# Optimization experiments

Measured on AMD Instinct MI355X. Metric: run time of the kernel, lower is better.

## Reference

```python
import jax, jax.numpy as jnp
from jax import lax
import numpy as np

H_AA = 20          # raw Potts alphabet
H_PAD = 22         # after (0,2) pad on both residue axes
EMB = H_PAD * H_PAD  # 484, LightAttention channel dim == MLP width
KSZ = 9            # LightAttention conv kernel


def setup_inputs() -> dict:
    key = jax.random.key(0)
    ks = jax.random.split(key, 16)
    b, n, k = 8, 512, 30
    S_mut = 99
    sc = 0.02
    inp = {
        'batch_etab': jax.random.normal(ks[0], (b, n, k, H_AA * H_AA), dtype=jnp.float32),
        'E_idx': jax.random.randint(ks[1], (b, n, k), 0, n),
        'sortcery_seqs': jax.random.randint(ks[2], (b, S_mut, n), 0, H_AA),
        'seqs': jax.random.randint(ks[3], (b, n), 0, H_AA),
        'mut_pos': jax.random.randint(ks[4], (b,), 0, n),
        'nodes': jnp.zeros((1,), dtype=jnp.float32),
        # LightAttention params (Conv1d: [out_ch, in_ch, ksz])
        'W_f': jax.random.normal(ks[5], (EMB, EMB, KSZ), dtype=jnp.float32) * sc,
        'b_f': jnp.zeros((EMB,), dtype=jnp.float32),
        'W_a': jax.random.normal(ks[6], (EMB, EMB, KSZ), dtype=jnp.float32) * sc,
        'b_a': jnp.zeros((EMB,), dtype=jnp.float32),
        # both_out: ReLU -> Linear(EMB,EMB) -> ReLU -> Linear(EMB,484)
        'W1': jax.random.normal(ks[7], (EMB, EMB), dtype=jnp.float32) * sc,
        'b1': jnp.zeros((EMB,), dtype=jnp.float32),
        'W2': jax.random.normal(ks[8], (EMB, EMB), dtype=jnp.float32) * sc,
        'b2': jnp.zeros((EMB,), dtype=jnp.float32),
        # ddg_out: Linear(1,1) -> scalar affine
        'w_ddg': jax.random.normal(ks[9], (1, 1), dtype=jnp.float32),
        'b_ddg': jnp.zeros((1,), dtype=jnp.float32),
    }
    return inp


def _conv1d_same(x, W, b):
    # x: [B, C, L], W: [O, I, K] -> [B, O, L] (stride 1, SAME pad for K=9)
    p = KSZ // 2
    y = lax.conv_general_dilated(x, W, (1,), [(p, p)],
                                 dimension_numbers=('NCH', 'OIH', 'NCH'))
    return y + b[None, :, None]


def reference(batch_etab, E_idx, sortcery_seqs, seqs, mut_pos, nodes,
              W_f, b_f, W_a, b_a, W1, b1, W2, b2, w_ddg, b_ddg):
    b, n, k, hh = batch_etab.shape
    h = H_AA
    # view (b,n,k,h,h), pad last two dims (0,2) each, flatten -> (b,n,k,484)
    e = batch_etab.reshape(b, n, k, h, h)
    e = jnp.pad(e, ((0, 0), (0, 0), (0, 0), (0, 2), (0, 2)))
    e = e.reshape(b, n, k, EMB)

    bidx = jnp.arange(b)
    # expand_etab_4d followed by [mut_pos] row-select == scatter the mut_pos
    # neighbor slab into a dense [n, EMB] row (avoids the full [n,n,EMB] dense).
    rows = e[bidx, mut_pos]          # [b, k, EMB]
    nbrs = E_idx[bidx, mut_pos]      # [b, k]
    lin = jnp.zeros((b, n, EMB), dtype=batch_etab.dtype)
    lin = lin.at[bidx[:, None], nbrs].set(rows)   # [b, n, EMB]

    mask = lin[:, :, 0] != 0                       # [b, n]

    # LightAttention (eval mode: dropout = identity)
    x = lin.transpose(0, 2, 1)                     # [b, EMB, n]
    o = _conv1d_same(x, W_f, b_f)
    att = _conv1d_same(x, W_a, b_a)
    att = jnp.where(mask[:, None, :], att, -1e9)
    o1 = o * jax.nn.softmax(att, axis=-1)          # [b, EMB, n]
    la = o1.transpose(0, 2, 1)                     # [b, n, EMB]

    # both_out: ReLU -> Linear -> ReLU -> Linear
    y = jax.nn.relu(la) @ W1.T + b1
    y = jax.nn.relu(y) @ W2.T + b2                 # [b, n, 484]
    # ddg_out Linear(1,1) applied elementwise on trailing singleton
    ddg = y * w_ddg[0, 0] + b_ddg[0]               # [b, n, 484]

    etab2 = ddg.reshape(b, n, H_PAD, H_PAD)        # [b, n, 22, 22]

    sort_seqs = jnp.concatenate([sortcery_seqs, seqs[:, None, :]], axis=1)  # [b,S,n]
    S = sort_seqs.shape[1]
    # batch_score_seq_batch_pos: score[b,s] = sum_j etab2[b, j, seq[mut_pos], seq[j]]
    s_pos = jnp.take_along_axis(sort_seqs, mut_pos[:, None, None], axis=2)[..., 0]  # [b,S]
    scores = etab2[bidx[:, None, None], jnp.arange(n)[None, None, :],
                   s_pos[:, :, None], sort_seqs].sum(axis=-1)  # [b, S]

    # subtract WT (last) score, drop WT row
    all_scores = (scores - scores[:, -1:])[:, :-1]             # [b, S-1]
    return all_scores
```

## Files before the change

### kernel.cpp

```cpp
#include <hip/hip_runtime.h>
#include <math.h>

#define H_AA   20
#define H_PAD  22
#define EMB    484
#define KSZ    9
#define NB     8
#define NPOS   512
#define KNBR   30
#define SMUT   99
#define STOT   100
#define ROWS   (NB*KNBR)
#define MROWS  241
#define NTOT   968
#define KC     400

__global__ void setup_kernel(const int* __restrict__ E_idx,
                             const int* __restrict__ mut_pos,
                             const float* __restrict__ etab,
                             int* __restrict__ rowidx_g,
                             int* __restrict__ mcount,
                             int* __restrict__ pairtap,
                             int* __restrict__ cnttap) {
    int b  = blockIdx.x;
    int mp = mut_pos[b];
    __shared__ int jmap[NPOS];
    __shared__ int wcnt[8], wbase[8];
    int t = threadIdx.x;
    jmap[t] = -1;
    __syncthreads();
    if (t < KNBR) {
        int nb = E_idx[(b * NPOS + mp) * KNBR + t];
        bool winner = true;
        for (int j2 = t + 1; j2 < KNBR; ++j2)
            if (E_idx[(b * NPOS + mp) * KNBR + j2] == nb) { winner = false; break; }
        if (winner) jmap[nb] = t;
    }
    __syncthreads();
    int j = jmap[t];
    int f = 0;
    if (j >= 0) {
        float c0 = etab[(((size_t)(b * NPOS + mp)) * KNBR + j) * 400];
        f = (c0 != 0.0f) ? 1 : 0;
    }
    unsigned long long bal = __ballot(f);
    int lane = t & 63, w = t >> 6;
    if (lane == 0) wcnt[w] = __popcll(bal);
    __syncthreads();
    if (t == 0) {
        int s = 0;
        for (int ww = 0; ww < 8; ++ww) { wbase[ww] = s; s += wcnt[ww]; }
        mcount[b] = s;
    }
    __syncthreads();
    int ridx = -1;
    if (f) ridx = wbase[w] + __popcll(bal & ((1ull << lane) - 1ull));
    rowidx_g[b * NPOS + t] = ridx;
    if (f) {
        int row = b * KNBR + ridx;
        for (int d = -4; d <= 4; ++d) {
            int q = t + d;
            if (q < 0 || q >= NPOS) continue;
            int jq = jmap[q];
            if (jq < 0) continue;
            int tap = d + 4;
            int idx = atomicAdd(&cnttap[tap], 1);
            pairtap[tap * 256 + idx] = (row << 5) | jq;
        }
    }
}

__global__ void pack_conv_kernel(const float* __restrict__ Wf,
                                 const float* __restrict__ Wa,
                                 float* __restrict__ Wp) {
    int half = blockIdx.z;
    const float* src = half ? Wa : Wf;
    int cb = blockIdx.x * 32;
    int ob = blockIdx.y * 32;
    __shared__ float tile[32][33];
    for (int yy = threadIdx.y; yy < 32; yy += 8) {
        int out = ob + yy, c = cb + threadIdx.x;
        if (out < EMB && c < EMB * KSZ)
            tile[yy][threadIdx.x] = src[(size_t)out * (EMB * KSZ) + c];
    }
    __syncthreads();
    for (int yy = threadIdx.y; yy < 32; yy += 8) {
        int c = cb + yy, out = ob + threadIdx.x;
        if (c < EMB * KSZ && out < EMB) {
            int tap = c % 9, in_pad = c / 9;
            int rr = in_pad / H_PAD, cc = in_pad % H_PAD;
            if (rr < H_AA && cc < H_AA) {
                int k = tap * KC + rr * H_AA + cc;
                Wp[(size_t)k * NTOT + half * EMB + out] = tile[threadIdx.x][yy];
            }
        }
    }
}

__global__ void transpose_lin_kernel(const float* __restrict__ W1,
                                     const float* __restrict__ W2,
                                     float* __restrict__ W1t,
                                     float* __restrict__ W2t) {
    const float* src = blockIdx.z ? W2 : W1;
    float*       dst = blockIdx.z ? W2t : W1t;
    __shared__ float tile[32][33];
    int c0 = blockIdx.x * 32, r0 = blockIdx.y * 32;
    for (int ty = threadIdx.y; ty < 32; ty += 8) {
        int r = r0 + ty, c = c0 + threadIdx.x;
        if (r < EMB && c < EMB) tile[ty][threadIdx.x] = src[(size_t)r * EMB + c];
    }
    __syncthreads();
    for (int ty = threadIdx.y; ty < 32; ty += 8) {
        int c = c0 + ty, r = r0 + threadIdx.x;
        if (r < EMB && c < EMB) dst[(size_t)c * EMB + r] = tile[threadIdx.x][ty];
    }
}

__global__ void conv_gemm_kernel(const float* __restrict__ etab,
                                 const float* __restrict__ Wp,
                                 const float* __restrict__ b_f,
                                 const float* __restrict__ b_a,
                                 const int* __restrict__ mut_pos,
                                 const int* __restrict__ pairtap,
                                 const int* __restrict__ cnttap,
                                 double* __restrict__ C) {
    int tap   = blockIdx.x / 15;
    int chunk = blockIdx.x % 15;
    int cnt = cnttap[tap];
    if (chunk * 16 >= cnt) return;
    int nt0 = blockIdx.y * 64;
    int t = threadIdx.x;
    int g = t >> 6, nl = t & 63;
    int n = nt0 + nl;

    __shared__ int   prow[16];
    __shared__ int   pbase[16];
    __shared__ float Ws[16][64];
    __shared__ float Xs[16][20];

    if (t < 16) {
        int idx = chunk * 16 + t;
        int pk = (idx < cnt) ? pairtap[tap * 256 + idx] : -1;
        int row = pk >> 5;
        prow[t] = (pk >= 0) ? row : -1;
        if (pk >= 0) {
            int b = row / KNBR;
            pbase[t] = ((b * NPOS + mut_pos[b]) * KNBR + (pk & 31)) * 400;
        } else pbase[t] = 0;
    }

    double binit = 0.0;
    if (tap == 4 && n < NTOT)
        binit = (double)(n < EMB ? b_f[n] : b_a[n - EMB]);
    double a0 = binit, a1 = binit, a2 = binit, a3 = binit;
    __syncthreads();

    int kkl = t >> 4, c4 = t & 15;
    for (int kb = 0; kb < KC; kb += 16) {
        {
            int nc = nt0 + c4 * 4;
            const float* wrow = Wp + (size_t)(tap * KC + kb + kkl) * NTOT;
            float4 w = make_float4(0.f, 0.f, 0.f, 0.f);
            if (nc + 3 < NTOT) w = *(const float4*)(wrow + nc);
            else {
                if (nc     < NTOT) w.x = wrow[nc];
                if (nc + 1 < NTOT) w.y = wrow[nc + 1];
                if (nc + 2 < NTOT) w.z = wrow[nc + 2];
            }
            *(float4*)&Ws[kkl][c4 * 4] = w;
        }
        {
            int m = t >> 4, kk = t & 15;
            int row = prow[m];
            float xv = 0.0f;
            if (row >= 0) xv = etab[(size_t)pbase[m] + kb + kk];
            Xs[kk][m] = xv;
        }
        __syncthreads();
        #pragma unroll
        for (int kk = 0; kk < 16; ++kk) {
            double w = (double)Ws[kk][nl];
            float4 x4 = *(const float4*)&Xs[kk][g * 4];
            a0 += w * (double)x4.x;
            a1 += w * (double)x4.y;
            a2 += w * (double)x4.z;
            a3 += w * (double)x4.w;
        }
        __syncthreads();
    }
    if (n < NTOT) {
        int r0 = prow[g * 4 + 0], r1 = prow[g * 4 + 1];
        int r2 = prow[g * 4 + 2], r3 = prow[g * 4 + 3];
        if (r0 >= 0) atomicAdd(&C[(size_t)r0 * NTOT + n], a0);
        if (r1 >= 0) atomicAdd(&C[(size_t)r1 * NTOT + n], a1);
        if (r2 >= 0) atomicAdd(&C[(size_t)r2 * NTOT + n], a2);
        if (r3 >= 0) atomicAdd(&C[(size_t)r3 * NTOT + n], a3);
    }
}

__global__ void softmax_kernel(const double* __restrict__ C,
                               const int* __restrict__ mcount,
                               float* __restrict__ la) {
    int idx = blockIdx.x * blockDim.x + threadIdx.x;
    if (idx >= NB * EMB) return;
    int b = idx / EMB, ch = idx % EMB;
    int m = mcount[b];
    if (m == 0) return;
    float mx = -1e30f;
    for (int i = 0; i < m; ++i)
        mx = fmaxf(mx, (float)C[(size_t)(b * KNBR + i) * NTOT + EMB + ch]);
    double sum = 0.0;
    for (int i = 0; i < m; ++i)
        sum += (double)expf((float)C[(size_t)(b * KNBR + i) * NTOT + EMB + ch] - mx);
    for (int i = 0; i < m; ++i) {
        size_t o = (size_t)(b * KNBR + i) * NTOT;
        float w = (float)((double)expf((float)C[o + EMB + ch] - mx) / sum);
        la[(size_t)(b * KNBR + i) * EMB + ch] = (float)C[o + ch] * w;
    }
}

__global__ void mlp_gemm_kernel(const float* __restrict__ X,
                                const float* __restrict__ Wt,
                                const float* __restrict__ bias,
                                const float* __restrict__ wdd,
                                const float* __restrict__ bdd,
                                float* __restrict__ Y, int mode) {
    int m0  = blockIdx.x * 16;
    int nt0 = blockIdx.y * 64;
    int t = threadIdx.x;
    int g = t >> 6, nl = t & 63;
    int n = nt0 + nl;
    __shared__ float Ws[16][64];
    __shared__ float Xs[16][20];
    double a0 = 0, a1 = 0, a2 = 0, a3 = 0;
    int kkl = t >> 4, c4 = t & 15;
    for (int kb = 0; kb < EMB; kb += 16) {
        {
            int k = kb + kkl;
            int nc = nt0 + c4 * 4;
            float4 w = make_float4(0.f, 0.f, 0.f, 0.f);
            if (k < EMB) {
                const float* wrow = Wt + (size_t)k * EMB;
                if (nc + 3 < EMB) w = *(const float4*)(wrow + nc);
                else {
                    if (nc     < EMB) w.x = wrow[nc];
                    if (nc + 1 < EMB) w.y = wrow[nc + 1];
                    if (nc + 2 < EMB) w.z = wrow[nc + 2];
                }
            }
            *(float4*)&Ws[kkl][c4 * 4] = w;
        }
        {
            int m = t >> 4, kk = t & 15;
            int row = m0 + m, k = kb + kk;
            float xv = 0.0f;
            if (row < MROWS && k < EMB)
                xv = fmaxf(X[(size_t)row * EMB + k], 0.0f);
            Xs[kk][m] = xv;
        }
        __syncthreads();
        #pragma unroll
        for (int kk = 0; kk < 16; ++kk) {
            double w = (double)Ws[kk][nl];
            float4 x4 = *(const float4*)&Xs[kk][g * 4];
            a0 += w * (double)x4.x;
            a1 += w * (double)x4.y;
            a2 += w * (double)x4.z;
            a3 += w * (double)x4.w;
        }
        __syncthreads();
    }
    if (n < EMB) {
        double bs = (double)bias[n];
        double acc[4] = {a0, a1, a2, a3};
        for (int r = 0; r < 4; ++r) {
            int row = m0 + g * 4 + r;
            if (row >= MROWS) continue;
            float v = (float)(acc[r] + bs);
            if (mode == 2) v = v * wdd[0] + bdd[0];
            Y[(size_t)row * EMB + n] = v;
        }
    }
}

__global__ void score_kernel(const int* __restrict__ sortc,
                             const int* __restrict__ seqs,
                             const int* __restrict__ mut_pos,
                             const int* __restrict__ rowidx,
                             const float* __restrict__ rows_all,
                             double* __restrict__ scoresD) {
    int blk = blockIdx.x;
    int b = blk / STOT, s = blk % STOT;
    int mp = mut_pos[b];
    int a = (s < SMUT) ? sortc[((size_t)b * SMUT + s) * NPOS + mp]
                       : seqs[b * NPOS + mp];
    int t = threadIdx.x;
    double acc = 0.0;
    for (int j = t; j < NPOS; j += 256) {
        int c = (s < SMUT) ? sortc[((size_t)b * SMUT + s) * NPOS + j]
                           : seqs[b * NPOS + j];
        int i = rowidx[b * NPOS + j];
        int row = (i >= 0) ? (b * KNBR + i) : (ROWS);
        acc += (double)rows_all[(size_t)row * EMB + a * H_PAD + c];
    }
    __shared__ double part[4];
    for (int off = 32; off > 0; off >>= 1)
        acc += __shfl_down(acc, off, 64);
    if ((t & 63) == 0) part[t >> 6] = acc;
    __syncthreads();
    if (t == 0) scoresD[blk] = part[0] + part[1] + part[2] + part[3];
}

__global__ void final_kernel(const double* __restrict__ scoresD,
                             float* __restrict__ out) {
    int idx = blockIdx.x * blockDim.x + threadIdx.x;
    if (idx >= NB * SMUT) return;
    int b = idx / SMUT, s = idx % SMUT;
    out[idx] = (float)(scoresD[b * STOT + s] - scoresD[b * STOT + SMUT]);
}

extern "C" void kernel_launch(void* const* d_in, const int* in_sizes, int n_in,
                              void* d_out, int out_size, void* d_ws, size_t ws_size,
                              hipStream_t stream) {
    const float* etab = (const float*)d_in[0];
    const int*   E_idx = (const int*)d_in[1];
    const int*   sortc = (const int*)d_in[2];
    const int*   seqs  = (const int*)d_in[3];
    const int*   mutp  = (const int*)d_in[4];
    const float* W_f = (const float*)d_in[6];
    const float* b_f = (const float*)d_in[7];
    const float* W_a = (const float*)d_in[8];
    const float* b_a = (const float*)d_in[9];
    const float* W1  = (const float*)d_in[10];
    const float* b1  = (const float*)d_in[11];
    const float* W2  = (const float*)d_in[12];
    const float* b2  = (const float*)d_in[13];
    const float* wdd = (const float*)d_in[14];
    const float* bdd = (const float*)d_in[15];
    float* out = (float*)d_out;

    char* wsb = (char*)d_ws;
    size_t off = 0;
    auto alloc = [&](size_t bytes) -> void* {
        void* p = wsb + off;
        off = (off + bytes + 255) & ~((size_t)255);
        return p;
    };
    double* C       = (double*)alloc((size_t)ROWS * NTOT * 8);
    float*  la_buf  = (float*)alloc((size_t)MROWS * EMB * 4);
    int*    cnttap  = (int*)alloc(9 * 4);
    size_t zbytes = off;
    float*  Wp      = (float*)alloc((size_t)9 * KC * NTOT * 4);
    float*  W1t     = (float*)alloc((size_t)EMB * EMB * 4);
    float*  W2t     = (float*)alloc((size_t)EMB * EMB * 4);
    int*    rowidx  = (int*)alloc((size_t)NB * NPOS * 4);
    int*    mcount  = (int*)alloc((size_t)NB * 4);
    int*    pairtap = (int*)alloc((size_t)9 * 256 * 4);
    float*  y1      = (float*)alloc((size_t)MROWS * EMB * 4);
    float*  rows_all= (float*)alloc((size_t)MROWS * EMB * 4);
    double* scoresD = (double*)alloc((size_t)NB * STOT * 8);
    (void)ws_size; (void)in_sizes; (void)n_in; (void)out_size;

    hipMemsetAsync(d_ws, 0, zbytes, stream);

    setup_kernel<<<NB, 512, 0, stream>>>(E_idx, mutp, etab, rowidx, mcount,
                                         pairtap, cnttap);

    {
        dim3 g((EMB * KSZ + 31) / 32, (EMB + 31) / 32, 2);
        pack_conv_kernel<<<g, dim3(32, 8), 0, stream>>>(W_f, W_a, Wp);
    }
    {
        dim3 g((EMB + 31) / 32, (EMB + 31) / 32, 2);
        transpose_lin_kernel<<<g, dim3(32, 8), 0, stream>>>(W1, W2, W1t, W2t);
    }

    conv_gemm_kernel<<<dim3(9 * 15, 16), 256, 0, stream>>>(etab, Wp, b_f, b_a,
                                                           mutp, pairtap, cnttap, C);
    softmax_kernel<<<(NB * EMB + 255) / 256, 256, 0, stream>>>(C, mcount, la_buf);
    mlp_gemm_kernel<<<dim3((MROWS + 15) / 16, (EMB + 63) / 64), 256, 0, stream>>>(
        la_buf, W1t, b1, wdd, bdd, y1, 1);
    mlp_gemm_kernel<<<dim3((MROWS + 15) / 16, (EMB + 63) / 64), 256, 0, stream>>>(
        y1, W2t, b2, wdd, bdd, rows_all, 2);
    score_kernel<<<NB * STOT, 256, 0, stream>>>(sortc, seqs, mutp, rowidx,
                                                rows_all, scoresD);
    final_kernel<<<(NB * SMUT + 255) / 256, 256, 0, stream>>>(scoresD, out);
}
```

Before: 424.8 us.

## Fuse weight prep and zeroing into one kernel; use fp32 accumulation in GEMMs

Merges the conv weight packing, linear weight transposes and workspace zeroing (previously a memset) into a single prep kernel, which cuts launches. The conv GEMM and the first MLP GEMM now accumulate in fp32 instead of fp64, and the conv bias is added at the atomic stage. FP64 FMA throughput is lower than FP32, so the main GEMMs should get cheaper. The cost is less precise accumulation, which could matter for the downstream score differences.

```diff
diff --git a/kernel.cpp b/kernel.cpp
--- a/kernel.cpp
+++ b/kernel.cpp
@@ -14,6 +14,67 @@
 #define MROWS  241
 #define NTOT   968
 #define KC     400
+#define PT_CAP 256
+#define NCHUNK 15
+
+__global__ void prep_kernel(const float* __restrict__ Wf,
+                            const float* __restrict__ Wa,
+                            float* __restrict__ Wp,
+                            const float* __restrict__ W1,
+                            const float* __restrict__ W2,
+                            float* __restrict__ W1t,
+                            float* __restrict__ W2t,
+                            double* __restrict__ C,
+                            float* __restrict__ la,
+                            int* __restrict__ cnttap) {
+    int z = blockIdx.z;
+    if (z < 2) {
+        const float* src = z ? Wa : Wf;
+        int cb = blockIdx.x * 32;
+        int ob = blockIdx.y * 32;
+        __shared__ float tile[32][33];
+        for (int yy = threadIdx.y; yy < 32; yy += 8) {
+            int out = ob + yy, c = cb + threadIdx.x;
+            if (out < EMB && c < EMB * KSZ)
+                tile[yy][threadIdx.x] = src[(size_t)out * (EMB * KSZ) + c];
+        }
+        __syncthreads();
+        for (int yy = threadIdx.y; yy < 32; yy += 8) {
+            int c = cb + yy, out = ob + threadIdx.x;
+            if (c < EMB * KSZ && out < EMB) {
+                int tap = c % 9, in_pad = c / 9;
+                int rr = in_pad / H_PAD, cc = in_pad % H_PAD;
+                if (rr < H_AA && cc < H_AA) {
+                    int k = tap * KC + rr * H_AA + cc;
+                    Wp[(size_t)k * NTOT + z * EMB + out] = tile[threadIdx.x][yy];
+                }
+            }
+        }
+    } else if (z < 4) {
+        if (blockIdx.x >= 16) return;
+        const float* src = (z == 3) ? W2 : W1;
+        float*       dst = (z == 3) ? W2t : W1t;
+        __shared__ float tile[32][33];
+        int c0 = blockIdx.x * 32, r0 = blockIdx.y * 32;
+        for (int ty = threadIdx.y; ty < 32; ty += 8) {
+            int r = r0 + ty, c = c0 + threadIdx.x;
+            if (r < EMB && c < EMB) tile[ty][threadIdx.x] = src[(size_t)r * EMB + c];
+        }
+        __syncthreads();
+        for (int ty = threadIdx.y; ty < 32; ty += 8) {
+            int c = c0 + ty, r = r0 + threadIdx.x;
+            if (r < EMB && c < EMB) dst[(size_t)c * EMB + r] = tile[threadIdx.x][ty];
+        }
+    } else {
+        size_t id = (((size_t)blockIdx.y * 137 + blockIdx.x) * 256)
+                    + threadIdx.y * 32 + threadIdx.x;
+        const size_t NC = (size_t)ROWS * NTOT;
+        const size_t NL = (size_t)MROWS * EMB;
+        if (id < NC) C[id] = 0.0;
+        else if (id < NC + NL) la[id - NC] = 0.0f;
+        if (id < 9) cnttap[id] = 0;
+    }
+}
 
 __global__ void setup_kernel(const int* __restrict__ E_idx,
                              const int* __restrict__ mut_pos,
@@ -65,54 +126,8 @@
             if (jq < 0) continue;
             int tap = d + 4;
             int idx = atomicAdd(&cnttap[tap], 1);
-            pairtap[tap * 256 + idx] = (row << 5) | jq;
-        }
-    }
-}
-
-__global__ void pack_conv_kernel(const float* __restrict__ Wf,
-                                 const float* __restrict__ Wa,
-                                 float* __restrict__ Wp) {
-    int half = blockIdx.z;
-    const float* src = half ? Wa : Wf;
-    int cb = blockIdx.x * 32;
-    int ob = blockIdx.y * 32;
-    __shared__ float tile[32][33];
-    for (int yy = threadIdx.y; yy < 32; yy += 8) {
-        int out = ob + yy, c = cb + threadIdx.x;
-        if (out < EMB && c < EMB * KSZ)
-            tile[yy][threadIdx.x] = src[(size_t)out * (EMB * KSZ) + c];
-    }
-    __syncthreads();
-    for (int yy = threadIdx.y; yy < 32; yy += 8) {
-        int c = cb + yy, out = ob + threadIdx.x;
-        if (c < EMB * KSZ && out < EMB) {
-            int tap = c % 9, in_pad = c / 9;
-            int rr = in_pad / H_PAD, cc = in_pad % H_PAD;
-            if (rr < H_AA && cc < H_AA) {
-                int k = tap * KC + rr * H_AA + cc;
-                Wp[(size_t)k * NTOT + half * EMB + out] = tile[threadIdx.x][yy];
-            }
-        }
-    }
-}
-
-__global__ void transpose_lin_kernel(const float* __restrict__ W1,
-                                     const float* __restrict__ W2,
-                                     float* __restrict__ W1t,
-                                     float* __restrict__ W2t) {
-    const float* src = blockIdx.z ? W2 : W1;
-    float*       dst = blockIdx.z ? W2t : W1t;
-    __shared__ float tile[32][33];
-    int c0 = blockIdx.x * 32, r0 = blockIdx.y * 32;
-    for (int ty = threadIdx.y; ty < 32; ty += 8) {
-        int r = r0 + ty, c = c0 + threadIdx.x;
-        if (r < EMB && c < EMB) tile[ty][threadIdx.x] = src[(size_t)r * EMB + c];
-    }
-    __syncthreads();
-    for (int ty = threadIdx.y; ty < 32; ty += 8) {
-        int c = c0 + ty, r = r0 + threadIdx.x;
-        if (r < EMB && c < EMB) dst[(size_t)c * EMB + r] = tile[threadIdx.x][ty];
+            pairtap[tap * PT_CAP + idx] = (row << 5) | jq;
+        }
     }
 }
 
@@ -124,8 +139,8 @@
                                  const int* __restrict__ pairtap,
                                  const int* __restrict__ cnttap,
                                  double* __restrict__ C) {
-    int tap   = blockIdx.x / 15;
-    int chunk = blockIdx.x % 15;
+    int tap   = blockIdx.x / NCHUNK;
+    int chunk = blockIdx.x % NCHUNK;
     int cnt = cnttap[tap];
     if (chunk * 16 >= cnt) return;
     int nt0 = blockIdx.y * 64;
@@ -140,7 +155,7 @@
 
     if (t < 16) {
         int idx = chunk * 16 + t;
-        int pk = (idx < cnt) ? pairtap[tap * 256 + idx] : -1;
+        int pk = (idx < cnt) ? pairtap[tap * PT_CAP + idx] : -1;
         int row = pk >> 5;
         prow[t] = (pk >= 0) ? row : -1;
         if (pk >= 0) {
@@ -148,11 +163,7 @@
             pbase[t] = ((b * NPOS + mut_pos[b]) * KNBR + (pk & 31)) * 400;
         } else pbase[t] = 0;
     }
-
-    double binit = 0.0;
-    if (tap == 4 && n < NTOT)
-        binit = (double)(n < EMB ? b_f[n] : b_a[n - EMB]);
-    double a0 = binit, a1 = binit, a2 = binit, a3 = binit;
+    float a0 = 0.f, a1 = 0.f, a2 = 0.f, a3 = 0.f;
     __syncthreads();
 
     int kkl = t >> 4, c4 = t & 15;
@@ -179,22 +190,23 @@
         __syncthreads();
         #pragma unroll
         for (int kk = 0; kk < 16; ++kk) {
-            double w = (double)Ws[kk][nl];
+            float w = Ws[kk][nl];
             float4 x4 = *(const float4*)&Xs[kk][g * 4];
-            a0 += w * (double)x4.x;
-            a1 += w * (double)x4.y;
-            a2 += w * (double)x4.z;
-            a3 += w * (double)x4.w;
+            a0 += w * x4.x; a1 += w * x4.y;
+            a2 += w * x4.z; a3 += w * x4.w;
         }
         __syncthreads();
     }
     if (n < NTOT) {
+        double binit = 0.0;
+        if (tap == 4)
+            binit = (double)(n < EMB ? b_f[n] : b_a[n - EMB]);
         int r0 = prow[g * 4 + 0], r1 = prow[g * 4 + 1];
         int r2 = prow[g * 4 + 2], r3 = prow[g * 4 + 3];
-        if (r0 >= 0) atomicAdd(&C[(size_t)r0 * NTOT + n], a0);
-        if (r1 >= 0) atomicAdd(&C[(size_t)r1 * NTOT + n], a1);
-        if (r2 >= 0) atomicAdd(&C[(size_t)r2 * NTOT + n], a2);
-        if (r3 >= 0) atomicAdd(&C[(size_t)r3 * NTOT + n], a3);
+        if (r0 >= 0) atomicAdd(&C[(size_t)r0 * NTOT + n], (double)a0 + binit);
+        if (r1 >= 0) atomicAdd(&C[(size_t)r1 * NTOT + n], (double)a1 + binit);
+        if (r2 >= 0) atomicAdd(&C[(size_t)r2 * NTOT + n], (double)a2 + binit);
+        if (r3 >= 0) atomicAdd(&C[(size_t)r3 * NTOT + n], (double)a3 + binit);
     }
 }
 
@@ -232,7 +244,8 @@
     int n = nt0 + nl;
     __shared__ float Ws[16][64];
     __shared__ float Xs[16][20];
-    double a0 = 0, a1 = 0, a2 = 0, a3 = 0;
+    double d0 = 0, d1 = 0, d2 = 0, d3 = 0;
+    float  f0 = 0, f1 = 0, f2 = 0, f3 = 0;
     int kkl = t >> 4, c4 = t & 15;
     for (int kb = 0; kb < EMB; kb += 16) {
         {
@@ -259,20 +272,30 @@
             Xs[kk][m] = xv;
         }
         __syncthreads();
-        #pragma unroll
-        for (int kk = 0; kk < 16; ++kk) {
-            double w = (double)Ws[kk][nl];
-            float4 x4 = *(const float4*)&Xs[kk][g * 4];
-            a0 += w * (double)x4.x;
-            a1 += w * (double)x4.y;
-            a2 += w * (double)x4.z;
-            a3 += w * (double)x4.w;
+        if (mode == 1) {
+            #pragma unroll
+            for (int kk = 0; kk < 16; ++kk) {
+                float w = Ws[kk][nl];
+                float4 x4 = *(const float4*)&Xs[kk][g * 4];
+                f0 += w * x4.x; f1 += w * x4.y;
+                f2 += w * x4.z; f3 += w * x4.w;
+            }
+        } else {
+            #pragma unroll
+            for (int kk = 0; kk < 16; ++kk) {
+                double w = (double)Ws[kk][nl];
+                float4 x4 = *(const float4*)&Xs[kk][g * 4];
+                d0 += w * (double)x4.x; d1 += w * (double)x4.y;
+                d2 += w * (double)x4.z; d3 += w * (double)x4.w;
+            }
         }
         __syncthreads();
     }
     if (n < EMB) {
         double bs = (double)bias[n];
-        double acc[4] = {a0, a1, a2, a3};
+        double acc[4];
+        if (mode == 1) { acc[0]=f0; acc[1]=f1; acc[2]=f2; acc[3]=f3; }
+        else           { acc[0]=d0; acc[1]=d1; acc[2]=d2; acc[3]=d3; }
         for (int r = 0; r < 4; ++r) {
             int row = m0 + g * 4 + r;
             if (row >= MROWS) continue;
@@ -349,34 +372,26 @@
     double* C       = (double*)alloc((size_t)ROWS * NTOT * 8);
     float*  la_buf  = (float*)alloc((size_t)MROWS * EMB * 4);
     int*    cnttap  = (int*)alloc(9 * 4);
-    size_t zbytes = off;
     float*  Wp      = (float*)alloc((size_t)9 * KC * NTOT * 4);
     float*  W1t     = (float*)alloc((size_t)EMB * EMB * 4);
     float*  W2t     = (float*)alloc((size_t)EMB * EMB * 4);
     int*    rowidx  = (int*)alloc((size_t)NB * NPOS * 4);
     int*    mcount  = (int*)alloc((size_t)NB * 4);
-    int*    pairtap = (int*)alloc((size_t)9 * 256 * 4);
+    int*    pairtap = (int*)alloc((size_t)9 * PT_CAP * 4);
     float*  y1      = (float*)alloc((size_t)MROWS * EMB * 4);
     float*  rows_all= (float*)alloc((size_t)MROWS * EMB * 4);
     double* scoresD = (double*)alloc((size_t)NB * STOT * 8);
     (void)ws_size; (void)in_sizes; (void)n_in; (void)out_size;
 
-    hipMemsetAsync(d_ws, 0, zbytes, stream);
-
+    {
+        dim3 g((EMB * KSZ + 31) / 32, 16, 5);
+        prep_kernel<<<g, dim3(32, 8), 0, stream>>>(W_f, W_a, Wp, W1, W2, W1t, W2t,
+                                                   C, la_buf, cnttap);
+    }
     setup_kernel<<<NB, 512, 0, stream>>>(E_idx, mutp, etab, rowidx, mcount,
                                          pairtap, cnttap);
-
-    {
-        dim3 g((EMB * KSZ + 31) / 32, (EMB + 31) / 32, 2);
-        pack_conv_kernel<<<g, dim3(32, 8), 0, stream>>>(W_f, W_a, Wp);
-    }
-    {
-        dim3 g((EMB + 31) / 32, (EMB + 31) / 32, 2);
-        transpose_lin_kernel<<<g, dim3(32, 8), 0, stream>>>(W1, W2, W1t, W2t);
-    }
-
-    conv_gemm_kernel<<<dim3(9 * 15, 16), 256, 0, stream>>>(etab, Wp, b_f, b_a,
-                                                           mutp, pairtap, cnttap, C);
+    conv_gemm_kernel<<<dim3(9 * NCHUNK, 16), 256, 0, stream>>>(etab, Wp, b_f, b_a,
+                                                               mutp, pairtap, cnttap, C);
     softmax_kernel<<<(NB * EMB + 255) / 256, 256, 0, stream>>>(C, mcount, la_buf);
     mlp_gemm_kernel<<<dim3((MROWS + 15) / 16, (EMB + 63) / 64), 256, 0, stream>>>(
         la_buf, W1t, b1, wdd, bdd, y1, 1);
```

Result: faster. 416.3 us (-2.0%).
